# Kernel optimization log

Measured on AMD Instinct MI355X. Metric: run time of the kernel, lower is better.

## Reference

```python
import jax, jax.numpy as jnp
import numpy as np

D_MODEL = 1024
N_QK = 32
D_QK = 32
N_OV = 2048
D_OV = 1
SEQ = 1024
BATCH = 2
VKV = 16
ROT_DIM = 32
ROT_BASE = 10000.0
SCALE = D_QK ** 0.5  # cfg.attn_scale default = sqrt(d_qk_head)


def _kaiming(k, shape, fan_in):
    # torch kaiming_normal_(mode='fan_in', nonlinearity='relu'): std = sqrt(2/fan_in)
    return jax.random.normal(k, shape, jnp.float32) * np.sqrt(2.0 / fan_in)


def setup_inputs() -> dict:
    key = jax.random.key(0)
    ks = jax.random.split(key, 7)
    return {
        'resid': jax.random.normal(ks[0], (BATCH, SEQ, D_MODEL), jnp.float32),
        'W_Q': _kaiming(ks[1], (N_QK, D_MODEL, D_QK), D_MODEL * D_QK),
        'W_K': _kaiming(ks[2], (N_QK, D_MODEL, D_QK), D_MODEL * D_QK),
        'W_V': _kaiming(ks[3], (N_OV, D_MODEL, D_OV), D_MODEL * D_OV),
        'W_O': _kaiming(ks[4], (N_OV, D_OV, D_MODEL), D_OV * D_MODEL),
        'b_Q': jnp.zeros((N_QK, D_QK), jnp.float32),
        'b_K': jnp.zeros((N_QK, D_QK), jnp.float32),
        'b_V': jnp.zeros((N_OV, D_OV), jnp.float32),
        'virtual_k': _kaiming(ks[5], (VKV, N_QK, D_QK), N_QK * D_QK),
        'virtual_v': jnp.zeros((VKV, N_OV, D_OV), jnp.float32),
    }


def _rotary_sin_cos(n_ctx, rd, base):
    # GPT-NeoX style (non-adjacent pairs): freq repeated as (2 d)
    pos = jnp.arange(n_ctx, dtype=jnp.float32)
    dim = jnp.arange(rd // 2, dtype=jnp.float32)
    freq = base ** (dim / (rd / 2))
    freq = jnp.concatenate([freq, freq])
    angles = pos[:, None] / freq[None, :]  # (n_ctx, rd)
    return jnp.sin(angles), jnp.cos(angles)


def _apply_rotary(x, sin, cos, rd):
    # x: (batch, seq, head, d_head)
    s = x.shape[1]
    x_rot, x_pass = x[..., :rd], x[..., rd:]
    flip = jnp.concatenate([-x_rot[..., rd // 2:], x_rot[..., :rd // 2]], axis=-1)
    rot = x_rot * cos[None, :s, None, :] + flip * sin[None, :s, None, :]
    return jnp.concatenate([rot, x_pass], axis=-1)


def reference(resid, W_Q, W_K, W_V, W_O, b_Q, b_K, b_V, virtual_k, virtual_v):
    b, s, _ = resid.shape
    # per-head QKV projections + biases
    q = jnp.einsum('bsm,hmd->bshd', resid, W_Q) + b_Q  # (b,s,n_qk,d_qk)
    k = jnp.einsum('bsm,hmd->bshd', resid, W_K) + b_K
    v = jnp.einsum('bsm,hmd->bshd', resid, W_V) + b_V  # (b,s,n_ov,d_ov)
    sin, cos = _rotary_sin_cos(s, ROT_DIM, ROT_BASE)
    q = _apply_rotary(q, sin, cos, ROT_DIM)
    k = _apply_rotary(k, sin, cos, ROT_DIM)
    # append virtual KV at the end of the key axis
    k = jnp.concatenate([k, jnp.broadcast_to(virtual_k[None], (b,) + virtual_k.shape)], axis=1)
    v = jnp.concatenate([v, jnp.broadcast_to(virtual_v[None], (b,) + virtual_v.shape)], axis=1)
    kv_len = s + VKV
    scores = jnp.einsum('bqhd,bkhd->bhqk', q, k) / SCALE
    # causal mask: tril(ones(n_ctx, n_ctx+vkv), diagonal=vkv)
    mask = jnp.arange(kv_len)[None, :] <= (jnp.arange(s)[:, None] + VKV)
    scores = jnp.where(mask[None, None], scores, -jnp.inf)
    pattern = jax.nn.softmax(scores, axis=-1)
    pattern = jnp.where(jnp.isnan(pattern), 0.0, pattern)
    # repeat_interleave of pattern over ov heads == grouping v per qk head
    ratio = N_OV // N_QK
    v_g = v.reshape(b, kv_len, N_QK, ratio * D_OV)
    z = jnp.einsum('bhqk,bkhr->bqhr', pattern, v_g)  # (b,s,n_qk,ratio*d_ov)
    z = z.reshape(b, s, N_OV, D_OV)
    out = jnp.einsum('bqhd,hdm->bqm', z, W_O)  # cal_out: no b_O
    return out
```

## Files before the change

kernel.cpp:

```cpp
#include <hip/hip_runtime.h>
#include <hip/hip_bf16.h>
#include <math.h>


typedef short bf16x8 __attribute__((ext_vector_type(8)));
typedef short short4v __attribute__((ext_vector_type(4)));
typedef float f32x4 __attribute__((ext_vector_type(4)));
typedef int int4v __attribute__((ext_vector_type(4)));
typedef __hip_bfloat16 bf16;

#define AS1(p) ((const __attribute__((address_space(1))) void*)(const void*)(p))
#define AS3(p) ((__attribute__((address_space(3))) void*)(void*)(p))

static constexpr float INV_SCALE = 0.17677669529663687f;

__device__ inline short rnd_bf16(float x) {
  unsigned u = __float_as_uint(x);
  return (short)((u + 0x7fffu + ((u >> 16) & 1u)) >> 16);
}

__device__ inline int pack_bf16_pair(float hi, float lo) {
  unsigned a = __float_as_uint(hi) + 0x8000u;
  unsigned b = __float_as_uint(lo) + 0x8000u;
  return (int)__builtin_amdgcn_perm(a, b, 0x07060302u);
}

__global__ __launch_bounds__(256) void prep(
    const float* __restrict__ resid, const float* __restrict__ WV,
    const float* __restrict__ WQ, const float* __restrict__ WK,
    const float* __restrict__ WO, const float* __restrict__ vk,
    const float* __restrict__ vv,
    bf16* __restrict__ A_bf, bf16* __restrict__ Wt, bf16* __restrict__ Wot,
    bf16* __restrict__ Kb, bf16* __restrict__ Vb) {
  __shared__ float t[64][65];
  const int blk = blockIdx.x, tid = threadIdx.x;
  if (blk < 4096) {
    const float* src = (blk < 2048) ? resid : WV;
    short* dst = (short*)((blk < 2048) ? A_bf : (Wt + (size_t)2048 * 1024));
    int i = ((blk & 2047) * 256 + tid) * 4;
    float4 v = *(const float4*)(src + i);
    dst[i + 0] = rnd_bf16(v.x); dst[i + 1] = rnd_bf16(v.y);
    dst[i + 2] = rnd_bf16(v.z); dst[i + 3] = rnd_bf16(v.w);
  } else if (blk < 7168) {
    int idx = (blk - 4096) * 256 + tid;
    if (idx < 262144) {
      int b = idx >> 17, rem = idx & 131071;
      int j = rem >> 10, c = rem & 1023;
      int h = c >> 5, d = c & 31;
      float v = (j < 16) ? vk[j * 1024 + c] : 0.f;
      Kb[(((size_t)(b * 32 + h)) * 1152 + 1024 + j) * 32 + d] = __float2bfloat16(v);
    } else if (idx < 524288) {
      int i2 = idx - 262144;
      int b = i2 >> 17, rem = i2 & 131071;
      int ch = rem >> 6, p = rem & 63;
      int pl = p & 31;
      int u = (p & 32) | ((pl & 4) << 2) | ((pl & 24) >> 1) | (pl & 3);
      float v = (u < 16) ? vv[(size_t)u * 2048 + ch] : 0.f;
      int hv = ch >> 6, c = ch & 63;
      int slot = c * 8 + ((p >> 3) ^ (c & 7));
      Vb[((((size_t)(b * 32 + hv)) * 17 + 16) * 512 + slot) * 8 + (p & 7)] = __float2bfloat16(v);
    }
  } else if (blk < 8192) {
    int i = blk - 7168;
    int mt = i & 15, h = (i >> 4) & 31, qk = i >> 9;
    const float* W = qk ? WK : WQ;
    const int m0 = mt * 64;
    for (int idx = tid; idx < 64 * 32; idx += 256) {
      int ii = idx >> 5, d = idx & 31;
      t[ii][d] = W[((size_t)h * 1024 + m0 + ii) * 32 + d];
    }
    __syncthreads();
    const int rowbase = qk * 1024 + h * 32;
    for (int idx = tid; idx < 32 * 64; idx += 256) {
      int d = idx >> 6, ii = idx & 63;
      Wt[(size_t)(rowbase + d) * 1024 + m0 + ii] = __float2bfloat16(t[ii][d]);
    }
  } else {
    int i = blk - 8192;
    int h0 = (i & 31) * 64, m0 = (i >> 5) * 64;
    for (int idx = tid; idx < 64 * 64; idx += 256) {
      int ii = idx >> 6, j = idx & 63;
      t[ii][j] = WO[(size_t)(h0 + ii) * 1024 + m0 + j];
    }
    __syncthreads();
    for (int idx = tid; idx < 64 * 64; idx += 256) {
      int ii = idx >> 6, j = idx & 63;
      Wot[(size_t)(m0 + ii) * 2048 + h0 + j] = __float2bfloat16(t[j][ii]);
    }
  }
}

__global__ __launch_bounds__(256) void gemm1_fused(
    const bf16* __restrict__ A, const bf16* __restrict__ Bt,
    const float* __restrict__ bQ, const float* __restrict__ bK,
    const float* __restrict__ bV,
    bf16* __restrict__ Qb, bf16* __restrict__ Kb, bf16* __restrict__ Vb) {
  __shared__ __align__(16) short As[128 * 32];
  __shared__ __align__(16) short Bs[128 * 32];
  const int flat = blockIdx.x;
  const int xcd = flat & 7, idx = flat >> 3;
  const int tileM = (xcd * 2 + (idx >> 5)) * 128;
  const int tileN = (idx & 31) * 128;
  const int tid = threadIdx.x, wave = tid >> 6, lane = tid & 63;
  const int wm = (wave >> 1) * 64, wn = (wave & 1) * 64;
  const int mrow = lane & 15, kq = lane >> 4;
  const bool isQK = tileN < 2048;
  f32x4 acc[4][4] = {};

  for (int k0 = 0; k0 < 1024; k0 += 32) {
#pragma unroll
    for (int i = 0; i < 2; i++) {
      int c = (wave * 2 + i) * 64 + lane;
      int row = c >> 2, ko = (c & 3) * 8;
      const short* ga = (const short*)A + (size_t)(tileM + row) * 1024 + k0 + ko;
      const short* gb = (const short*)Bt + (size_t)(tileN + row) * 1024 + k0 + ko;
      __builtin_amdgcn_global_load_lds(AS1(ga), AS3(&As[(wave * 2 + i) * 512]), 16, 0, 0);
      __builtin_amdgcn_global_load_lds(AS1(gb), AS3(&Bs[(wave * 2 + i) * 512]), 16, 0, 0);
    }
    __syncthreads();
    bf16x8 af[4], bfr[4];
#pragma unroll
    for (int t = 0; t < 4; t++) {
      af[t]  = *(const bf16x8*)&As[(wm + t * 16 + mrow) * 32 + kq * 8];
      bfr[t] = *(const bf16x8*)&Bs[(wn + t * 16 + mrow) * 32 + kq * 8];
    }
    if (isQK) {
#pragma unroll
      for (int fj = 0; fj < 4; fj++)
#pragma unroll
        for (int ti = 0; ti < 4; ti++)
          acc[fj][ti] = __builtin_amdgcn_mfma_f32_16x16x32_bf16(bfr[fj], af[ti], acc[fj][ti], 0, 0, 0);
    } else {
#pragma unroll
      for (int i = 0; i < 4; i++)
#pragma unroll
        for (int j = 0; j < 4; j++)
          acc[i][j] = __builtin_amdgcn_mfma_f32_16x16x32_bf16(af[i], bfr[j], acc[i][j], 0, 0, 0);
    }
    __syncthreads();
  }

  const int col = lane & 15, rq = lane >> 4;
  if (isQK) {
    const int qk = tileN >> 10;
    const float* bias = qk ? bK : bQ;
    const int hA = ((tileN & 1023) + wn) >> 5;
    const int d0 = rq * 4;
    const float4 bA0 = *(const float4*)&bias[hA * 32 + d0];
    const float4 bA1 = *(const float4*)&bias[hA * 32 + 16 + d0];
    const float4 bB0 = *(const float4*)&bias[(hA + 1) * 32 + d0];
    const float4 bB1 = *(const float4*)&bias[(hA + 1) * 32 + 16 + d0];
    float invf[4];
#pragma unroll
    for (int r = 0; r < 4; r++)
      invf[r] = exp2f((d0 + r) * -0.8304820237218406f);
    const float osc = qk ? 1.f : INV_SCALE;
#pragma unroll
    for (int ti = 0; ti < 4; ti++) {
      int sg = tileM + wm + ti * 16 + col;
      int s = sg & 1023, bb = sg >> 10;
      float sv[4], cv[4];
#pragma unroll
      for (int r = 0; r < 4; r++) __sincosf((float)s * invf[r], &sv[r], &cv[r]);
#pragma unroll
      for (int p = 0; p < 2; p++) {
        int h = hA + p;
        short4v z0, z1;
#pragma unroll
        for (int r = 0; r < 4; r++) {
          float x0 = acc[2 * p][ti][r]     + (p ? (&bB0.x)[r] : (&bA0.x)[r]);
          float x1 = acc[2 * p + 1][ti][r] + (p ? (&bB1.x)[r] : (&bA1.x)[r]);
          float y0 = (x0 * cv[r] - x1 * sv[r]) * osc;
          float y1 = (x1 * cv[r] + x0 * sv[r]) * osc;
          z0[r] = rnd_bf16(y0); z1[r] = rnd_bf16(y1);
        }
        short* dst = qk
            ? (short*)Kb + ((size_t)(bb * 32 + h) * 1152 + s) * 32
            : (short*)Qb + ((size_t)(bb * 32 + h) * 1024 + s) * 32;
        *(short4v*)(dst + d0) = z0;
        *(short4v*)(dst + 16 + d0) = z1;
      }
    }
  } else {
    const int hv = (tileN - 2048 + wn) >> 6;
#pragma unroll
    for (int i = 0; i < 4; i++)
#pragma unroll
      for (int j = 0; j < 4; j++) {
        int c = j * 16 + col;
        float bias = bV[hv * 64 + c];
        int m0 = tileM + wm + i * 16 + rq * 4;
        int s0 = m0 & 1023, bb = m0 >> 10;
        int chunk = s0 >> 6, w = s0 & 63, u0 = w & 31;
        int p0 = (u0 & 3) | ((u0 & 16) >> 2) | ((u0 & 8) << 1) | ((u0 & 4) << 1);
        int p = (w & 32) | p0;
        int slot = c * 8 + ((p >> 3) ^ (c & 7));
        short4v s4;
#pragma unroll
        for (int r = 0; r < 4; r++) s4[r] = rnd_bf16(acc[i][j][r] + bias);
        *(short4v*)((short*)Vb +
            ((((size_t)(bb * 32 + hv)) * 17 + chunk) * 512 + slot) * 8 + (p & 7)) = s4;
      }
  }
}

__global__ __launch_bounds__(256) void attn_mfma(
    const bf16* __restrict__ Qb, const bf16* __restrict__ Kb,
    const bf16* __restrict__ Vb, bf16* __restrict__ Zb) {
  __shared__ __align__(16) short Vs[4][4096];
  const int flat = blockIdx.x;
  const int xcd = flat & 7, jj = flat >> 3;
  const int hqb = xcd * 8 + (jj & 7);
  const int x = jj >> 3;
  const int hq = hqb & 31, b = hqb >> 5;
  const int wave = threadIdx.x >> 6, lane = threadIdx.x & 63;
  const int col = lane & 15, quad = lane >> 4;
  const int t = (wave == 0) ? x : (wave == 1) ? 31 - x : (wave == 2) ? 32 + x : 63 - x;
  const int qw = t * 16;

  const bf16x8 qf = *(const bf16x8*)((const short*)Qb +
      (((size_t)(b * 32 + hq)) * 1024 + qw + col) * 32 + quad * 8);
  const short* kbase = (const short*)Kb + ((size_t)(b * 32 + hq)) * 1152 * 32 + quad * 8;
  const short* vbh = (const short*)Vb + ((size_t)(b * 32 + hq)) * (17 * 4096) + lane * 8;
  short* vdst = &Vs[wave][0];

  const int kend = (qw + 32 < 1040) ? qw + 32 : 1040;
  const int nch = (kend + 63) >> 6;

  f32x4 O[4] = {};
  float m = -1e30f, l = 0.f;

  bf16x8 kf[4];
#pragma unroll
  for (int mbk = 0; mbk < 4; mbk++)
    kf[mbk] = *(const bf16x8*)(kbase + (size_t)(mbk * 16 + col) * 32);
#pragma unroll
  for (int g = 0; g < 8; g++)
    __builtin_amdgcn_global_load_lds(AS1(vbh + g * 512), AS3(vdst + g * 512), 16, 0, 0);

  for (int ci = 0; ci < nch; ci++) {
    const int kc = ci * 64;
    f32x4 St[4] = {};
#pragma unroll
    for (int mbk = 0; mbk < 4; mbk++)
      St[mbk] = __builtin_amdgcn_mfma_f32_16x16x32_bf16(kf[mbk], qf, St[mbk], 0, 0, 0);
    if (kc + 63 > qw + 16) {
      int qv = qw + col + 16;
#pragma unroll
      for (int mbk = 0; mbk < 4; mbk++)
#pragma unroll
        for (int r = 0; r < 4; r++)
          if (kc + mbk * 16 + quad * 4 + r > qv) St[mbk][r] = -1e30f;
    }
    float cm0 = fmaxf(fmaxf(St[0][0], St[0][1]), fmaxf(St[0][2], St[0][3]));
    float cm1 = fmaxf(fmaxf(St[1][0], St[1][1]), fmaxf(St[1][2], St[1][3]));
    float cm2 = fmaxf(fmaxf(St[2][0], St[2][1]), fmaxf(St[2][2], St[2][3]));
    float cm3 = fmaxf(fmaxf(St[3][0], St[3][1]), fmaxf(St[3][2], St[3][3]));
    float cmax = fmaxf(fmaxf(cm0, cm1), fmaxf(cm2, cm3));
    cmax = fmaxf(cmax, __shfl_xor(cmax, 16));
    cmax = fmaxf(cmax, __shfl_xor(cmax, 32));
    float mn = fmaxf(m, cmax);
    float al = __expf(m - mn);
    m = mn;
    float ps = 0.f;
#pragma unroll
    for (int mbk = 0; mbk < 4; mbk++)
#pragma unroll
      for (int r = 0; r < 4; r++) {
        float p = __expf(St[mbk][r] - mn);
        ps += p;
        St[mbk][r] = p;
      }
    ps += __shfl_xor(ps, 16);
    ps += __shfl_xor(ps, 32);
    l = l * al + ps;
    int4v pi[2];
#pragma unroll
    for (int pr = 0; pr < 2; pr++)
#pragma unroll
      for (int d = 0; d < 4; d++)
        pi[pr][d] = pack_bf16_pair(St[2 * pr + (d >> 1)][(d & 1) * 2 + 1],
                                   St[2 * pr + (d >> 1)][(d & 1) * 2]);
#pragma unroll
    for (int cb = 0; cb < 4; cb++)
#pragma unroll
      for (int r = 0; r < 4; r++) O[cb][r] *= al;
    asm volatile("s_waitcnt vmcnt(0)" ::: "memory");
    bf16x8 vf[2][4];
#pragma unroll
    for (int ks = 0; ks < 2; ks++)
#pragma unroll
      for (int cb = 0; cb < 4; cb++) {
        int slot = (cb * 16 + col) * 8 + ((ks * 4 + quad) ^ (col & 7));
        vf[ks][cb] = *(const bf16x8*)(vdst + slot * 8);
      }
    asm volatile("s_waitcnt lgkmcnt(0)" ::: "memory");
    if (ci + 1 < nch) {
      const int kn = kc + 64;
#pragma unroll
      for (int mbk = 0; mbk < 4; mbk++)
        kf[mbk] = *(const bf16x8*)(kbase + (size_t)(kn + mbk * 16 + col) * 32);
      const short* vsrc = vbh + (ci + 1) * 4096;
#pragma unroll
      for (int g = 0; g < 8; g++)
        __builtin_amdgcn_global_load_lds(AS1(vsrc + g * 512), AS3(vdst + g * 512), 16, 0, 0);
    }
#pragma unroll
    for (int ks = 0; ks < 2; ks++) {
      bf16x8 prs = *(bf16x8*)&pi[ks];
#pragma unroll
      for (int cb = 0; cb < 4; cb++)
        O[cb] = __builtin_amdgcn_mfma_f32_16x16x32_bf16(vf[ks][cb], prs, O[cb], 0, 0, 0);
    }
  }
  float inv = 1.f / l;
  short* zrow = (short*)Zb + ((size_t)(b * 1024 + qw + col)) * 2048 + hq * 64 + quad * 4;
#pragma unroll
  for (int cb = 0; cb < 4; cb++) {
    short4v s4;
#pragma unroll
    for (int r = 0; r < 4; r++) s4[r] = rnd_bf16(O[cb][r] * inv);
    *(short4v*)(zrow + cb * 16) = s4;
  }
}

__global__ __launch_bounds__(256) void gemm2_wide(
    const bf16* __restrict__ A, const bf16* __restrict__ Bt, float* __restrict__ C) {
  __shared__ __align__(16) short As[128 * 32];
  __shared__ __align__(16) short Bs[64 * 32];
  const int flat = blockIdx.x;
  const int xcd = flat & 7, idx = flat >> 3;
  const int tileM = (xcd * 2 + (idx >> 4)) * 128;
  const int tileN = (idx & 15) * 64;
  const int tid = threadIdx.x, wave = tid >> 6, lane = tid & 63;
  const int wm = (wave >> 1) * 64, wn = (wave & 1) * 32;
  const int mrow = lane & 15, kq = lane >> 4;
  f32x4 acc[4][2] = {};

  for (int k0 = 0; k0 < 2048; k0 += 32) {
#pragma unroll
    for (int i = 0; i < 2; i++) {
      int c = (wave * 2 + i) * 64 + lane;
      int row = c >> 2, ko = (c & 3) * 8;
      const short* ga = (const short*)A + (size_t)(tileM + row) * 2048 + k0 + ko;
      __builtin_amdgcn_global_load_lds(AS1(ga), AS3(&As[(wave * 2 + i) * 512]), 16, 0, 0);
    }
    {
      int c = wave * 64 + lane;
      int row = c >> 2, ko = (c & 3) * 8;
      const short* gb = (const short*)Bt + (size_t)(tileN + row) * 2048 + k0 + ko;
      __builtin_amdgcn_global_load_lds(AS1(gb), AS3(&Bs[wave * 512]), 16, 0, 0);
    }
    __syncthreads();
    bf16x8 af[4], bfr[2];
#pragma unroll
    for (int t = 0; t < 4; t++) af[t] = *(const bf16x8*)&As[(wm + t * 16 + mrow) * 32 + kq * 8];
#pragma unroll
    for (int t = 0; t < 2; t++) bfr[t] = *(const bf16x8*)&Bs[(wn + t * 16 + mrow) * 32 + kq * 8];
#pragma unroll
    for (int i = 0; i < 4; i++)
#pragma unroll
      for (int j = 0; j < 2; j++)
        acc[i][j] = __builtin_amdgcn_mfma_f32_16x16x32_bf16(af[i], bfr[j], acc[i][j], 0, 0, 0);
    __syncthreads();
  }
  const int col = lane & 15, rq = lane >> 4;
#pragma unroll
  for (int i = 0; i < 4; i++)
#pragma unroll
    for (int j = 0; j < 2; j++)
#pragma unroll
      for (int r = 0; r < 4; r++) {
        int mm = tileM + wm + i * 16 + rq * 4 + r;
        int nn = tileN + wn + j * 16 + col;
        C[(size_t)mm * 1024 + nn] = acc[i][j][r];
      }
}

extern "C" void kernel_launch(void* const* d_in, const int* in_sizes, int n_in,
                              void* d_out, int out_size, void* d_ws, size_t ws_size,
                              hipStream_t stream) {
  const float* resid = (const float*)d_in[0];
  const float* WQ = (const float*)d_in[1];
  const float* WK = (const float*)d_in[2];
  const float* WV = (const float*)d_in[3];
  const float* WO = (const float*)d_in[4];
  const float* bQ = (const float*)d_in[5];
  const float* bK = (const float*)d_in[6];
  const float* bV = (const float*)d_in[7];
  const float* vk = (const float*)d_in[8];
  const float* vv = (const float*)d_in[9];
  float* out = (float*)d_out;

  char* ws = (char*)d_ws;
  bf16* A_bf = (bf16*)(ws);
  bf16* Wt   = (bf16*)(ws + 4194304);
  bf16* Wot  = (bf16*)(ws + 12582912);
  bf16* Qb   = (bf16*)(ws + 16777216);
  bf16* Kb   = (bf16*)(ws + 20971520);
  bf16* Vb   = (bf16*)(ws + 25690112);
  bf16* Zb   = (bf16*)(ws + 35127296);

  prep<<<8704, 256, 0, stream>>>(resid, WV, WQ, WK, WO, vk, vv, A_bf, Wt, Wot, Kb, Vb);
  gemm1_fused<<<512, 256, 0, stream>>>(A_bf, Wt, bQ, bK, bV, Qb, Kb, Vb);
  attn_mfma<<<1024, 256, 0, stream>>>(Qb, Kb, Vb, Zb);
  gemm2_wide<<<256, 256, 0, stream>>>(Zb, Wot, out);
}
```

Before: 183.7 us.

## Pair complementary query tiles per wave in attention and shrink output GEMM tiles

Each attention wave now handles two query tiles, one near the start and one near the end of the sequence, so causal work is balanced and each loaded K/V chunk serves both tiles. V staging in LDS becomes double-buffered, which removes the wait on LDS reads before the next chunk is prefetched. The attention grid is halved to 512 blocks. The output projection switches to 64x64 tiles on a 2D grid of 512 blocks, trading per-block reuse for more parallelism. Doubling the accumulators and the LDS footprint may reduce occupancy.

```diff
diff --git a/kernel.cpp b/kernel.cpp
--- a/kernel.cpp
+++ b/kernel.cpp
@@ -207,158 +207,235 @@
 __global__ __launch_bounds__(256) void attn_mfma(
     const bf16* __restrict__ Qb, const bf16* __restrict__ Kb,
     const bf16* __restrict__ Vb, bf16* __restrict__ Zb) {
-  __shared__ __align__(16) short Vs[4][4096];
+  __shared__ __align__(16) short Vs[4][2][4096];
   const int flat = blockIdx.x;
-  const int xcd = flat & 7, jj = flat >> 3;
-  const int hqb = xcd * 8 + (jj & 7);
-  const int x = jj >> 3;
+  const int xcd = flat & 7;
+  const int hqb = xcd * 8 + ((flat >> 3) & 7);
+  const int xblk = flat >> 6;
   const int hq = hqb & 31, b = hqb >> 5;
   const int wave = threadIdx.x >> 6, lane = threadIdx.x & 63;
   const int col = lane & 15, quad = lane >> 4;
-  const int t = (wave == 0) ? x : (wave == 1) ? 31 - x : (wave == 2) ? 32 + x : 63 - x;
-  const int qw = t * 16;
-
-  const bf16x8 qf = *(const bf16x8*)((const short*)Qb +
-      (((size_t)(b * 32 + hq)) * 1024 + qw + col) * 32 + quad * 8);
+  const int pairIdx = xblk * 4 + wave;
+  const int qwA = pairIdx * 16, qwB = (63 - pairIdx) * 16;
+
+  const short* qbase = (const short*)Qb + ((size_t)(b * 32 + hq)) * 1024 * 32;
+  const bf16x8 qfA = *(const bf16x8*)(qbase + (qwA + col) * 32 + quad * 8);
+  const bf16x8 qfB = *(const bf16x8*)(qbase + (qwB + col) * 32 + quad * 8);
   const short* kbase = (const short*)Kb + ((size_t)(b * 32 + hq)) * 1152 * 32 + quad * 8;
   const short* vbh = (const short*)Vb + ((size_t)(b * 32 + hq)) * (17 * 4096) + lane * 8;
-  short* vdst = &Vs[wave][0];
-
-  const int kend = (qw + 32 < 1040) ? qw + 32 : 1040;
-  const int nch = (kend + 63) >> 6;
-
-  f32x4 O[4] = {};
-  float m = -1e30f, l = 0.f;
+
+  const int kendA = qwA + 32;
+  const int nchA = (kendA + 63) >> 6;
+  const int kendB = (qwB + 32 < 1040) ? qwB + 32 : 1040;
+  const int nchB = (kendB + 63) >> 6;
+
+  f32x4 OA[4] = {}, OB[4] = {};
+  float mA = -1e30f, lA = 0.f, mB = -1e30f, lB = 0.f;
 
   bf16x8 kf[4];
 #pragma unroll
   for (int mbk = 0; mbk < 4; mbk++)
     kf[mbk] = *(const bf16x8*)(kbase + (size_t)(mbk * 16 + col) * 32);
-#pragma unroll
-  for (int g = 0; g < 8; g++)
-    __builtin_amdgcn_global_load_lds(AS1(vbh + g * 512), AS3(vdst + g * 512), 16, 0, 0);
-
-  for (int ci = 0; ci < nch; ci++) {
+  {
+    short* vd = &Vs[wave][0][0];
+#pragma unroll
+    for (int g = 0; g < 8; g++)
+      __builtin_amdgcn_global_load_lds(AS1(vbh + g * 512), AS3(vd + g * 512), 16, 0, 0);
+  }
+
+  for (int ci = 0; ci < nchB; ci++) {
     const int kc = ci * 64;
-    f32x4 St[4] = {};
+    const bool aAct = ci < nchA;
+    f32x4 SB[4] = {};
 #pragma unroll
     for (int mbk = 0; mbk < 4; mbk++)
-      St[mbk] = __builtin_amdgcn_mfma_f32_16x16x32_bf16(kf[mbk], qf, St[mbk], 0, 0, 0);
-    if (kc + 63 > qw + 16) {
-      int qv = qw + col + 16;
+      SB[mbk] = __builtin_amdgcn_mfma_f32_16x16x32_bf16(kf[mbk], qfB, SB[mbk], 0, 0, 0);
+    f32x4 SA[4] = {};
+    if (aAct) {
+#pragma unroll
+      for (int mbk = 0; mbk < 4; mbk++)
+        SA[mbk] = __builtin_amdgcn_mfma_f32_16x16x32_bf16(kf[mbk], qfA, SA[mbk], 0, 0, 0);
+    }
+    if (kc + 63 > qwB + 16) {
+      int qv = qwB + col + 16;
 #pragma unroll
       for (int mbk = 0; mbk < 4; mbk++)
 #pragma unroll
         for (int r = 0; r < 4; r++)
-          if (kc + mbk * 16 + quad * 4 + r > qv) St[mbk][r] = -1e30f;
-    }
-    float cm0 = fmaxf(fmaxf(St[0][0], St[0][1]), fmaxf(St[0][2], St[0][3]));
-    float cm1 = fmaxf(fmaxf(St[1][0], St[1][1]), fmaxf(St[1][2], St[1][3]));
-    float cm2 = fmaxf(fmaxf(St[2][0], St[2][1]), fmaxf(St[2][2], St[2][3]));
-    float cm3 = fmaxf(fmaxf(St[3][0], St[3][1]), fmaxf(St[3][2], St[3][3]));
-    float cmax = fmaxf(fmaxf(cm0, cm1), fmaxf(cm2, cm3));
-    cmax = fmaxf(cmax, __shfl_xor(cmax, 16));
-    cmax = fmaxf(cmax, __shfl_xor(cmax, 32));
-    float mn = fmaxf(m, cmax);
-    float al = __expf(m - mn);
-    m = mn;
-    float ps = 0.f;
-#pragma unroll
-    for (int mbk = 0; mbk < 4; mbk++)
-#pragma unroll
-      for (int r = 0; r < 4; r++) {
-        float p = __expf(St[mbk][r] - mn);
-        ps += p;
-        St[mbk][r] = p;
-      }
-    ps += __shfl_xor(ps, 16);
-    ps += __shfl_xor(ps, 32);
-    l = l * al + ps;
-    int4v pi[2];
-#pragma unroll
-    for (int pr = 0; pr < 2; pr++)
-#pragma unroll
-      for (int d = 0; d < 4; d++)
-        pi[pr][d] = pack_bf16_pair(St[2 * pr + (d >> 1)][(d & 1) * 2 + 1],
-                                   St[2 * pr + (d >> 1)][(d & 1) * 2]);
-#pragma unroll
-    for (int cb = 0; cb < 4; cb++)
-#pragma unroll
-      for (int r = 0; r < 4; r++) O[cb][r] *= al;
+          if (kc + mbk * 16 + quad * 4 + r > qv) SB[mbk][r] = -1e30f;
+    }
+    if (aAct && kc + 63 > qwA + 16) {
+      int qv = qwA + col + 16;
+#pragma unroll
+      for (int mbk = 0; mbk < 4; mbk++)
+#pragma unroll
+        for (int r = 0; r < 4; r++)
+          if (kc + mbk * 16 + quad * 4 + r > qv) SA[mbk][r] = -1e30f;
+    }
+    int4v piB[2], piA[2];
+    {
+      float c0 = fmaxf(fmaxf(SB[0][0], SB[0][1]), fmaxf(SB[0][2], SB[0][3]));
+      float c1 = fmaxf(fmaxf(SB[1][0], SB[1][1]), fmaxf(SB[1][2], SB[1][3]));
+      float c2 = fmaxf(fmaxf(SB[2][0], SB[2][1]), fmaxf(SB[2][2], SB[2][3]));
+      float c3 = fmaxf(fmaxf(SB[3][0], SB[3][1]), fmaxf(SB[3][2], SB[3][3]));
+      float cmax = fmaxf(fmaxf(c0, c1), fmaxf(c2, c3));
+      cmax = fmaxf(cmax, __shfl_xor(cmax, 16));
+      cmax = fmaxf(cmax, __shfl_xor(cmax, 32));
+      float mn = fmaxf(mB, cmax);
+      float al = __expf(mB - mn);
+      mB = mn;
+      float ps = 0.f;
+#pragma unroll
+      for (int mbk = 0; mbk < 4; mbk++)
+#pragma unroll
+        for (int r = 0; r < 4; r++) {
+          float p = __expf(SB[mbk][r] - mn);
+          ps += p;
+          SB[mbk][r] = p;
+        }
+      ps += __shfl_xor(ps, 16);
+      ps += __shfl_xor(ps, 32);
+      lB = lB * al + ps;
+#pragma unroll
+      for (int pr = 0; pr < 2; pr++)
+#pragma unroll
+        for (int d = 0; d < 4; d++)
+          piB[pr][d] = pack_bf16_pair(SB[2 * pr + (d >> 1)][(d & 1) * 2 + 1],
+                                      SB[2 * pr + (d >> 1)][(d & 1) * 2]);
+#pragma unroll
+      for (int cb = 0; cb < 4; cb++)
+#pragma unroll
+        for (int r = 0; r < 4; r++) OB[cb][r] *= al;
+    }
+    if (aAct) {
+      float c0 = fmaxf(fmaxf(SA[0][0], SA[0][1]), fmaxf(SA[0][2], SA[0][3]));
+      float c1 = fmaxf(fmaxf(SA[1][0], SA[1][1]), fmaxf(SA[1][2], SA[1][3]));
+      float c2 = fmaxf(fmaxf(SA[2][0], SA[2][1]), fmaxf(SA[2][2], SA[2][3]));
+      float c3 = fmaxf(fmaxf(SA[3][0], SA[3][1]), fmaxf(SA[3][2], SA[3][3]));
+      float cmax = fmaxf(fmaxf(c0, c1), fmaxf(c2, c3));
+      cmax = fmaxf(cmax, __shfl_xor(cmax, 16));
+      cmax = fmaxf(cmax, __shfl_xor(cmax, 32));
+      float mn = fmaxf(mA, cmax);
+      float al = __expf(mA - mn);
+      mA = mn;
+      float ps = 0.f;
+#pragma unroll
+      for (int mbk = 0; mbk < 4; mbk++)
+#pragma unroll
+        for (int r = 0; r < 4; r++) {
+          float p = __expf(SA[mbk][r] - mn);
+          ps += p;
+          SA[mbk][r] = p;
+        }
+      ps += __shfl_xor(ps, 16);
+      ps += __shfl_xor(ps, 32);
+      lA = lA * al + ps;
+#pragma unroll
+      for (int pr = 0; pr < 2; pr++)
+#pragma unroll
+        for (int d = 0; d < 4; d++)
+          piA[pr][d] = pack_bf16_pair(SA[2 * pr + (d >> 1)][(d & 1) * 2 + 1],
+                                      SA[2 * pr + (d >> 1)][(d & 1) * 2]);
+#pragma unroll
+      for (int cb = 0; cb < 4; cb++)
+#pragma unroll
+        for (int r = 0; r < 4; r++) OA[cb][r] *= al;
+    }
     asm volatile("s_waitcnt vmcnt(0)" ::: "memory");
+    const short* vd = &Vs[wave][ci & 1][0];
     bf16x8 vf[2][4];
 #pragma unroll
     for (int ks = 0; ks < 2; ks++)
 #pragma unroll
       for (int cb = 0; cb < 4; cb++) {
         int slot = (cb * 16 + col) * 8 + ((ks * 4 + quad) ^ (col & 7));
-        vf[ks][cb] = *(const bf16x8*)(vdst + slot * 8);
+        vf[ks][cb] = *(const bf16x8*)(vd + slot * 8);
       }
-    asm volatile("s_waitcnt lgkmcnt(0)" ::: "memory");
-    if (ci + 1 < nch) {
+    if (ci + 1 < nchB) {
       const int kn = kc + 64;
 #pragma unroll
       for (int mbk = 0; mbk < 4; mbk++)
         kf[mbk] = *(const bf16x8*)(kbase + (size_t)(kn + mbk * 16 + col) * 32);
       const short* vsrc = vbh + (ci + 1) * 4096;
+      short* vdn = &Vs[wave][(ci + 1) & 1][0];
 #pragma unroll
       for (int g = 0; g < 8; g++)
-        __builtin_amdgcn_global_load_lds(AS1(vsrc + g * 512), AS3(vdst + g * 512), 16, 0, 0);
+        __builtin_amdgcn_global_load_lds(AS1(vsrc + g * 512), AS3(vdn + g * 512), 16, 0, 0);
     }
 #pragma unroll
     for (int ks = 0; ks < 2; ks++) {
-      bf16x8 prs = *(bf16x8*)&pi[ks];
+      bf16x8 prB = *(bf16x8*)&piB[ks];
 #pragma unroll
       for (int cb = 0; cb < 4; cb++)
-        O[cb] = __builtin_amdgcn_mfma_f32_16x16x32_bf16(vf[ks][cb], prs, O[cb], 0, 0, 0);
-    }
-  }
-  float inv = 1.f / l;
-  short* zrow = (short*)Zb + ((size_t)(b * 1024 + qw + col)) * 2048 + hq * 64 + quad * 4;
-#pragma unroll
-  for (int cb = 0; cb < 4; cb++) {
-    short4v s4;
-#pragma unroll
-    for (int r = 0; r < 4; r++) s4[r] = rnd_bf16(O[cb][r] * inv);
-    *(short4v*)(zrow + cb * 16) = s4;
-  }
-}
-
-__global__ __launch_bounds__(256) void gemm2_wide(
-    const bf16* __restrict__ A, const bf16* __restrict__ Bt, float* __restrict__ C) {
-  __shared__ __align__(16) short As[128 * 32];
+        OB[cb] = __builtin_amdgcn_mfma_f32_16x16x32_bf16(vf[ks][cb], prB, OB[cb], 0, 0, 0);
+    }
+    if (aAct) {
+#pragma unroll
+      for (int ks = 0; ks < 2; ks++) {
+        bf16x8 prA = *(bf16x8*)&piA[ks];
+#pragma unroll
+        for (int cb = 0; cb < 4; cb++)
+          OA[cb] = __builtin_amdgcn_mfma_f32_16x16x32_bf16(vf[ks][cb], prA, OA[cb], 0, 0, 0);
+      }
+    }
+  }
+  {
+    float inv = 1.f / lA;
+    short* zrow = (short*)Zb + ((size_t)(b * 1024 + qwA + col)) * 2048 + hq * 64 + quad * 4;
+#pragma unroll
+    for (int cb = 0; cb < 4; cb++) {
+      short4v s4;
+#pragma unroll
+      for (int r = 0; r < 4; r++) s4[r] = rnd_bf16(OA[cb][r] * inv);
+      *(short4v*)(zrow + cb * 16) = s4;
+    }
+  }
+  {
+    float inv = 1.f / lB;
+    short* zrow = (short*)Zb + ((size_t)(b * 1024 + qwB + col)) * 2048 + hq * 64 + quad * 4;
+#pragma unroll
+    for (int cb = 0; cb < 4; cb++) {
+      short4v s4;
+#pragma unroll
+      for (int r = 0; r < 4; r++) s4[r] = rnd_bf16(OB[cb][r] * inv);
+      *(short4v*)(zrow + cb * 16) = s4;
+    }
+  }
+}
+
+__global__ __launch_bounds__(256) void gemm2_small(
+    const bf16* __restrict__ A, const bf16* __restrict__ Bt, float* __restrict__ C,
+    int K, int ldc) {
+  __shared__ __align__(16) short As[64 * 32];
   __shared__ __align__(16) short Bs[64 * 32];
-  const int flat = blockIdx.x;
-  const int xcd = flat & 7, idx = flat >> 3;
-  const int tileM = (xcd * 2 + (idx >> 4)) * 128;
-  const int tileN = (idx & 15) * 64;
+  const int tileM = blockIdx.y * 64, tileN = blockIdx.x * 64;
   const int tid = threadIdx.x, wave = tid >> 6, lane = tid & 63;
-  const int wm = (wave >> 1) * 64, wn = (wave & 1) * 32;
+  const int wm = (wave >> 1) * 32, wn = (wave & 1) * 32;
   const int mrow = lane & 15, kq = lane >> 4;
-  f32x4 acc[4][2] = {};
-
-  for (int k0 = 0; k0 < 2048; k0 += 32) {
-#pragma unroll
-    for (int i = 0; i < 2; i++) {
-      int c = (wave * 2 + i) * 64 + lane;
-      int row = c >> 2, ko = (c & 3) * 8;
-      const short* ga = (const short*)A + (size_t)(tileM + row) * 2048 + k0 + ko;
-      __builtin_amdgcn_global_load_lds(AS1(ga), AS3(&As[(wave * 2 + i) * 512]), 16, 0, 0);
-    }
+  f32x4 acc[2][2] = {};
+
+  for (int k0 = 0; k0 < K; k0 += 32) {
     {
       int c = wave * 64 + lane;
       int row = c >> 2, ko = (c & 3) * 8;
-      const short* gb = (const short*)Bt + (size_t)(tileN + row) * 2048 + k0 + ko;
+      const short* ga = (const short*)A + (size_t)(tileM + row) * K + k0 + ko;
+      __builtin_amdgcn_global_load_lds(AS1(ga), AS3(&As[wave * 512]), 16, 0, 0);
+    }
+    {
+      int c = wave * 64 + lane;
+      int row = c >> 2, ko = (c & 3) * 8;
+      const short* gb = (const short*)Bt + (size_t)(tileN + row) * K + k0 + ko;
       __builtin_amdgcn_global_load_lds(AS1(gb), AS3(&Bs[wave * 512]), 16, 0, 0);
     }
     __syncthreads();
-    bf16x8 af[4], bfr[2];
-#pragma unroll
-    for (int t = 0; t < 4; t++) af[t] = *(const bf16x8*)&As[(wm + t * 16 + mrow) * 32 + kq * 8];
-#pragma unroll
-    for (int t = 0; t < 2; t++) bfr[t] = *(const bf16x8*)&Bs[(wn + t * 16 + mrow) * 32 + kq * 8];
-#pragma unroll
-    for (int i = 0; i < 4; i++)
+    bf16x8 af[2], bfr[2];
+#pragma unroll
+    for (int t = 0; t < 2; t++) {
+      af[t]  = *(const bf16x8*)&As[(wm + t * 16 + mrow) * 32 + kq * 8];
+      bfr[t] = *(const bf16x8*)&Bs[(wn + t * 16 + mrow) * 32 + kq * 8];
+    }
+#pragma unroll
+    for (int i = 0; i < 2; i++)
 #pragma unroll
       for (int j = 0; j < 2; j++)
         acc[i][j] = __builtin_amdgcn_mfma_f32_16x16x32_bf16(af[i], bfr[j], acc[i][j], 0, 0, 0);
@@ -366,14 +443,14 @@
   }
   const int col = lane & 15, rq = lane >> 4;
 #pragma unroll
-  for (int i = 0; i < 4; i++)
+  for (int i = 0; i < 2; i++)
 #pragma unroll
     for (int j = 0; j < 2; j++)
 #pragma unroll
       for (int r = 0; r < 4; r++) {
         int mm = tileM + wm + i * 16 + rq * 4 + r;
         int nn = tileN + wn + j * 16 + col;
-        C[(size_t)mm * 1024 + nn] = acc[i][j][r];
+        C[(size_t)mm * ldc + nn] = acc[i][j][r];
       }
 }
 
@@ -403,6 +480,6 @@
 
   prep<<<8704, 256, 0, stream>>>(resid, WV, WQ, WK, WO, vk, vv, A_bf, Wt, Wot, Kb, Vb);
   gemm1_fused<<<512, 256, 0, stream>>>(A_bf, Wt, bQ, bK, bV, Qb, Kb, Vb);
-  attn_mfma<<<1024, 256, 0, stream>>>(Qb, Kb, Vb, Zb);
-  gemm2_wide<<<256, 256, 0, stream>>>(Zb, Wot, out);
-}
+  attn_mfma<<<512, 256, 0, stream>>>(Qb, Kb, Vb, Zb);
+  gemm2_small<<<dim3(16, 32), 256, 0, stream>>>(Zb, Wot, out, 2048, 1024);
+}
```

New measurement: 175.2 us. 1.05x faster.
